# Kernel optimization log

Hardware: AMD Instinct MI355X
Metric: run time of the kernel (lower is better)

The kernel has to match this reference:

```python
import jax, jax.numpy as jnp
import numpy as np

N_NODES = 100000
N_EDGES = 1250000
D_IN = 64
D_HID = 64
N_CLS = 40


def setup_inputs() -> dict:
    key = jax.random.key(0)
    ks = jax.random.split(key, 8)
    x = jax.random.normal(ks[0], (N_NODES, D_IN), dtype=jnp.float32)
    edge_index = jax.random.randint(ks[1], (2, N_EDGES), 0, N_NODES, dtype=jnp.int64)
    s = 1.0 / np.sqrt(D_IN)
    W1_l = jax.random.normal(ks[2], (D_IN, D_HID), dtype=jnp.float32) * s
    W1_r = jax.random.normal(ks[3], (D_IN, D_HID), dtype=jnp.float32) * s
    b1 = jnp.zeros((D_HID,), dtype=jnp.float32)
    s2 = 1.0 / np.sqrt(D_HID)
    W2_l = jax.random.normal(ks[4], (D_HID, N_CLS), dtype=jnp.float32) * s2
    W2_r = jax.random.normal(ks[5], (D_HID, N_CLS), dtype=jnp.float32) * s2
    b2 = jnp.zeros((N_CLS,), dtype=jnp.float32)
    return {"x": x, "edge_index": edge_index, "W1_l": W1_l, "b1": b1,
            "W1_r": W1_r, "W2_l": W2_l, "b2": b2, "W2_r": W2_r}


def _sage_conv(h, src, dst, n_nodes, W_l, b, W_r):
    # mean-aggregate neighbor features: out[i] = mean_{(j->i)} h[j]
    msg = h[src]                                             # [E, d] gather
    agg = jax.ops.segment_sum(msg, dst, num_segments=n_nodes)  # [N, d] scatter-add
    deg = jax.ops.segment_sum(jnp.ones_like(dst, dtype=h.dtype), dst,
                              num_segments=n_nodes)
    agg = agg / jnp.maximum(deg, 1.0)[:, None]
    # lin_l(aggregated, bias) + lin_r(root, no bias)
    return agg @ W_l + b + h @ W_r


def reference(x, edge_index, W1_l, b1, W1_r, W2_l, b2, W2_r):
    n = x.shape[0]
    src, dst = edge_index[0], edge_index[1]
    h = jax.nn.relu(_sage_conv(x, src, dst, n, W1_l, b1, W1_r))
    # dropout is identity in eval mode (training=False)
    h = _sage_conv(h, src, dst, n, W2_l, b2, W2_r)
    return jax.nn.log_softmax(h, axis=1)
```

## Files before the change

kernel.cpp:

```cpp
#include <hip/hip_runtime.h>
#include <hip/hip_bf16.h>
#include <math.h>

#define N_NODES 100000
#define N_EDGES 1250000
#define D_IN    64
#define D_HID   64
#define N_CLS   40

#define NBUCK      500
#define BUCK_NODES 200
#define BUCK_CAP   2944
#define NBLK_STAGE 512
#define ELL_W      44

typedef unsigned int uint;
typedef __attribute__((ext_vector_type(8))) short bf16x8;
typedef __attribute__((ext_vector_type(4))) float f32x4;

static __device__ __forceinline__ uint pack_bf16x2(float a, float b) {
    unsigned short ua = __builtin_bit_cast(unsigned short, __float2bfloat16(a));
    unsigned short ub = __builtin_bit_cast(unsigned short, __float2bfloat16(b));
    return (uint)ua | ((uint)ub << 16);
}
static __device__ __forceinline__ short f2bf(float f) {
    return (short)__builtin_bit_cast(unsigned short, __float2bfloat16(f));
}

__global__ __launch_bounds__(256) void bucket_stage(
    const int* __restrict__ src, const int* __restrict__ dst,
    int* __restrict__ bucketCnt, uint* __restrict__ staged, int n_edges)
{
    __shared__ int cntB[NBUCK], offB[NBUCK], gbase[NBUCK];
    const int per = (n_edges + NBLK_STAGE - 1) / NBLK_STAGE;
    const int e0 = blockIdx.x * per;
    const int e1 = (e0 + per < n_edges) ? e0 + per : n_edges;
    for (int i = threadIdx.x; i < NBUCK; i += 256) { cntB[i] = 0; offB[i] = 0; }
    __syncthreads();
    for (int e = e0 + threadIdx.x; e < e1; e += 256)
        atomicAdd(&cntB[dst[e] / BUCK_NODES], 1);
    __syncthreads();
    for (int i = threadIdx.x; i < NBUCK; i += 256) {
        int c = cntB[i];
        gbase[i] = c ? atomicAdd(&bucketCnt[i], c) : 0;
    }
    __syncthreads();
    for (int e = e0 + threadIdx.x; e < e1; e += 256) {
        int d = dst[e];
        int s = src[e];
        int b = d / BUCK_NODES;
        int pos = gbase[b] + atomicAdd(&offB[b], 1);
        if (pos < BUCK_CAP)
            staged[(size_t)b * BUCK_CAP + pos] =
                (uint)s | ((uint)(d - b * BUCK_NODES) << 17);
    }
}

__global__ __launch_bounds__(256) void ell_fill(
    const uint* __restrict__ staged, const int* __restrict__ bucketCnt,
    int* __restrict__ cnt, int* __restrict__ slots)
{
    __shared__ int lcnt[BUCK_NODES];
    const int b = blockIdx.x;
    const int node0 = b * BUCK_NODES;
    for (int i = threadIdx.x; i < BUCK_NODES; i += 256) lcnt[i] = 0;
    __syncthreads();
    int total = bucketCnt[b];
    if (total > BUCK_CAP) total = BUCK_CAP;
    const uint* sp = staged + (size_t)b * BUCK_CAP;
    for (int i = threadIdx.x; i < total; i += 256) {
        uint v = sp[i];
        int off = (int)(v >> 17);
        int pos = atomicAdd(&lcnt[off], 1);
        if (pos < ELL_W)
            slots[(size_t)(node0 + off) * ELL_W + pos] = (int)(v & 0x1FFFFu);
    }
    __syncthreads();
    for (int i = threadIdx.x; i < BUCK_NODES; i += 256) {
        int node = node0 + i;
        if (node < N_NODES) cnt[node] = lcnt[i];
    }
}

__global__ __launch_bounds__(256, 3) void gemm1_mfma(
    const float* __restrict__ x,
    const float* __restrict__ W_l, const float* __restrict__ W_r,
    const float* __restrict__ b,
    __hip_bfloat16* __restrict__ y1, __hip_bfloat16* __restrict__ r1,
    int ntiles)
{
    const int lane = threadIdx.x & 63;
    const int m = lane & 15;
    const int q = lane >> 4;

    bf16x8 bfrag[8][2];
    float  biasv[4];
    #pragma unroll
    for (int t = 0; t < 8; ++t) {
        const float* Wsrc = (t < 4) ? W_l : W_r;
        const int c = t * 16 + m - ((t < 4) ? 0 : 64);
        #pragma unroll
        for (int ks = 0; ks < 2; ++ks) {
            bf16x8 f;
            #pragma unroll
            for (int j = 0; j < 8; ++j)
                f[j] = f2bf(Wsrc[(ks * 32 + q * 8 + j) * 64 + c]);
            bfrag[t][ks] = f;
        }
    }
    #pragma unroll
    for (int t = 0; t < 4; ++t) biasv[t] = b[t * 16 + m];

    int wid = blockIdx.x * 4 + (threadIdx.x >> 6);
    const int nw = gridDim.x * 4;
    for (int tile = wid; tile < ntiles; tile += nw) {
        const int node0 = tile * 16;
        const float* xrow = x + (size_t)(node0 + m) * 64 + q * 8;
        bf16x8 afrag[2];
        #pragma unroll
        for (int ks = 0; ks < 2; ++ks) {
            float4 f0 = *(const float4*)(xrow + ks * 32);
            float4 f1 = *(const float4*)(xrow + ks * 32 + 4);
            bf16x8 a;
            a[0] = f2bf(f0.x); a[1] = f2bf(f0.y); a[2] = f2bf(f0.z); a[3] = f2bf(f0.w);
            a[4] = f2bf(f1.x); a[5] = f2bf(f1.y); a[6] = f2bf(f1.z); a[7] = f2bf(f1.w);
            afrag[ks] = a;
        }
        f32x4 acc[8];
        #pragma unroll
        for (int t = 0; t < 8; ++t) acc[t] = (f32x4){0.f, 0.f, 0.f, 0.f};
        #pragma unroll
        for (int ks = 0; ks < 2; ++ks) {
            #pragma unroll
            for (int t = 0; t < 8; ++t)
                acc[t] = __builtin_amdgcn_mfma_f32_16x16x32_bf16(
                    afrag[ks], bfrag[t][ks], acc[t], 0, 0, 0);
        }
        #pragma unroll
        for (int t = 0; t < 8; ++t) {
            #pragma unroll
            for (int r = 0; r < 4; ++r) {
                const size_t row = (size_t)(node0 + q * 4 + r);
                if (t < 4)
                    y1[row * 64 + t * 16 + m] = __float2bfloat16(acc[t][r]);
                else
                    r1[row * 64 + (t - 4) * 16 + m] =
                        __float2bfloat16(acc[t][r] + biasv[t - 4]);
            }
        }
    }
}

__global__ __launch_bounds__(256, 3) void gemm2_mfma(
    const __hip_bfloat16* __restrict__ h,
    const float* __restrict__ W_l, const float* __restrict__ W_r,
    const float* __restrict__ b,
    __hip_bfloat16* __restrict__ y2, __hip_bfloat16* __restrict__ r2,
    int ntiles)
{
    const int lane = threadIdx.x & 63;
    const int m = lane & 15;
    const int q = lane >> 4;

    bf16x8 bfrag[5][2];
    float  biasv[5];
    #pragma unroll
    for (int t = 0; t < 5; ++t) {
        const int g = t * 16 + m;
        const float* Wsrc = (g < N_CLS) ? W_l : W_r;
        const int c = (g < N_CLS) ? g : g - N_CLS;
        #pragma unroll
        for (int ks = 0; ks < 2; ++ks) {
            bf16x8 f;
            #pragma unroll
            for (int j = 0; j < 8; ++j)
                f[j] = f2bf(Wsrc[(ks * 32 + q * 8 + j) * N_CLS + c]);
            bfrag[t][ks] = f;
        }
        biasv[t] = (g >= N_CLS) ? b[g - N_CLS] : 0.0f;
    }

    int wid = blockIdx.x * 4 + (threadIdx.x >> 6);
    const int nw = gridDim.x * 4;
    for (int tile = wid; tile < ntiles; tile += nw) {
        const int node0 = tile * 16;
        const __hip_bfloat16* hrow = h + (size_t)(node0 + m) * 64 + q * 8;
        bf16x8 afrag[2];
        afrag[0] = *(const bf16x8*)(hrow);
        afrag[1] = *(const bf16x8*)(hrow + 32);
        f32x4 acc[5];
        #pragma unroll
        for (int t = 0; t < 5; ++t) acc[t] = (f32x4){0.f, 0.f, 0.f, 0.f};
        #pragma unroll
        for (int ks = 0; ks < 2; ++ks) {
            #pragma unroll
            for (int t = 0; t < 5; ++t)
                acc[t] = __builtin_amdgcn_mfma_f32_16x16x32_bf16(
                    afrag[ks], bfrag[t][ks], acc[t], 0, 0, 0);
        }
        #pragma unroll
        for (int t = 0; t < 5; ++t) {
            const int g = t * 16 + m;
            #pragma unroll
            for (int r = 0; r < 4; ++r) {
                const size_t row = (size_t)(node0 + q * 4 + r);
                float v = acc[t][r] + biasv[t];
                if (g < N_CLS) y2[row * N_CLS + g] = __float2bfloat16(v);
                else           r2[row * N_CLS + (g - N_CLS)] = __float2bfloat16(v);
            }
        }
    }
}

__global__ __launch_bounds__(256, 8) void gather1(
    const __hip_bfloat16* __restrict__ y1,
    const int* __restrict__ cnt, const int* __restrict__ slots,
    __hip_bfloat16* __restrict__ h,
    int n_nodes)
{
    const int lane = threadIdx.x & 63;
    const int q4  = (lane >> 4) * 4;
    const int pre = (lane & 15) * 8;
    const char* y1c = (const char*)y1;

    const int wave = blockIdx.x * 4 + (threadIdx.x >> 6);
    const int nw   = gridDim.x * 4;

    for (int node = wave; node < n_nodes; node += nw) {
        const int degr = cnt[node];
        const int degc = degr < ELL_W ? degr : ELL_W;
        int idx = slots[node * ELL_W + lane];
        if (lane >= degc) idx = n_nodes;
        float a0 = 0.f, a1 = 0.f, a2 = 0.f, a3 = 0.f;
        const int groups = (degc + 15) & ~15;
        for (int e = 0; e < groups; e += 16) {
            int sel0 = __builtin_amdgcn_ds_bpermute(e * 4      + q4, idx);
            int sel1 = __builtin_amdgcn_ds_bpermute(e * 4 + 16 + q4, idx);
            int sel2 = __builtin_amdgcn_ds_bpermute(e * 4 + 32 + q4, idx);
            int sel3 = __builtin_amdgcn_ds_bpermute(e * 4 + 48 + q4, idx);
            uint2 d0 = *(const uint2*)(y1c + ((size_t)(uint)sel0 * 128u + (uint)pre));
            uint2 d1 = *(const uint2*)(y1c + ((size_t)(uint)sel1 * 128u + (uint)pre));
            uint2 d2 = *(const uint2*)(y1c + ((size_t)(uint)sel2 * 128u + (uint)pre));
            uint2 d3 = *(const uint2*)(y1c + ((size_t)(uint)sel3 * 128u + (uint)pre));
            a0 += __uint_as_float(d0.x << 16) + __uint_as_float(d1.x << 16)
                + __uint_as_float(d2.x << 16) + __uint_as_float(d3.x << 16);
            a1 += __uint_as_float(d0.x & 0xffff0000u) + __uint_as_float(d1.x & 0xffff0000u)
                + __uint_as_float(d2.x & 0xffff0000u) + __uint_as_float(d3.x & 0xffff0000u);
            a2 += __uint_as_float(d0.y << 16) + __uint_as_float(d1.y << 16)
                + __uint_as_float(d2.y << 16) + __uint_as_float(d3.y << 16);
            a3 += __uint_as_float(d0.y & 0xffff0000u) + __uint_as_float(d1.y & 0xffff0000u)
                + __uint_as_float(d2.y & 0xffff0000u) + __uint_as_float(d3.y & 0xffff0000u);
        }
        a0 += __shfl_xor(a0, 16); a0 += __shfl_xor(a0, 32);
        a1 += __shfl_xor(a1, 16); a1 += __shfl_xor(a1, 32);
        a2 += __shfl_xor(a2, 16); a2 += __shfl_xor(a2, 32);
        a3 += __shfl_xor(a3, 16); a3 += __shfl_xor(a3, 32);

        uint2 rr = *(const uint2*)((const char*)h + ((size_t)node * 128u + (uint)pre));
        float r0  = __uint_as_float(rr.x << 16);
        float r1v = __uint_as_float(rr.x & 0xffff0000u);
        float r2v = __uint_as_float(rr.y << 16);
        float r3  = __uint_as_float(rr.y & 0xffff0000u);

        float inv = 1.0f / (float)(degr > 1 ? degr : 1);
        float v0 = a0 * inv + r0;  v0 = v0 > 0.f ? v0 : 0.f;
        float v1 = a1 * inv + r1v; v1 = v1 > 0.f ? v1 : 0.f;
        float v2 = a2 * inv + r2v; v2 = v2 > 0.f ? v2 : 0.f;
        float v3 = a3 * inv + r3;  v3 = v3 > 0.f ? v3 : 0.f;

        if (lane < 16) {
            uint2 o;
            o.x = pack_bf16x2(v0, v1);
            o.y = pack_bf16x2(v2, v3);
            *(uint2*)((char*)h + ((size_t)node * 128u + (uint)pre)) = o;
        }
    }
}

__global__ __launch_bounds__(256, 8) void gather2(
    const __hip_bfloat16* __restrict__ y2,
    const __hip_bfloat16* __restrict__ r2,
    const int* __restrict__ cnt, const int* __restrict__ slots,
    float* __restrict__ out, int n_nodes)
{
    const int lane  = threadIdx.x & 63;
    const int lpair = lane & 31;
    const int p2    = (lane >> 5) * 4;
    const int pre2  = (lpair < 20 ? lpair : 19) * 4;
    const char* y2c = (const char*)y2;

    const int wave = blockIdx.x * 4 + (threadIdx.x >> 6);
    const int nw   = gridDim.x * 4;

    for (int node = wave; node < n_nodes; node += nw) {
        const int degr = cnt[node];
        const int degc = degr < ELL_W ? degr : ELL_W;
        int idx = slots[node * ELL_W + lane];
        if (lane >= degc) idx = n_nodes;
        float a0 = 0.f, a1 = 0.f;
        const int groups = (degc + 7) & ~7;
        for (int e = 0; e < groups; e += 8) {
            int sel0 = __builtin_amdgcn_ds_bpermute(e * 4      + p2, idx);
            int sel1 = __builtin_amdgcn_ds_bpermute(e * 4 +  8 + p2, idx);
            int sel2 = __builtin_amdgcn_ds_bpermute(e * 4 + 16 + p2, idx);
            int sel3 = __builtin_amdgcn_ds_bpermute(e * 4 + 24 + p2, idx);
            uint d0 = *(const uint*)(y2c + ((size_t)(uint)sel0 * 80u + (uint)pre2));
            uint d1 = *(const uint*)(y2c + ((size_t)(uint)sel1 * 80u + (uint)pre2));
            uint d2 = *(const uint*)(y2c + ((size_t)(uint)sel2 * 80u + (uint)pre2));
            uint d3 = *(const uint*)(y2c + ((size_t)(uint)sel3 * 80u + (uint)pre2));
            a0 += __uint_as_float(d0 << 16) + __uint_as_float(d1 << 16)
                + __uint_as_float(d2 << 16) + __uint_as_float(d3 << 16);
            a1 += __uint_as_float(d0 & 0xffff0000u) + __uint_as_float(d1 & 0xffff0000u)
                + __uint_as_float(d2 & 0xffff0000u) + __uint_as_float(d3 & 0xffff0000u);
        }
        a0 += __shfl_xor(a0, 32);
        a1 += __shfl_xor(a1, 32);

        uint rr = *(const uint*)((const char*)r2 + ((size_t)node * 80u + (uint)pre2));
        float r0 = __uint_as_float(rr << 16);
        float r1 = __uint_as_float(rr & 0xffff0000u);

        float inv = 1.0f / (float)(degr > 1 ? degr : 1);
        float l0 = a0 * inv + r0;
        float l1 = a1 * inv + r1;
        if (lpair >= 20) { l0 = -INFINITY; l1 = -INFINITY; }

        float m = fmaxf(l0, l1);
        #pragma unroll
        for (int off = 16; off > 0; off >>= 1)
            m = fmaxf(m, __shfl_xor(m, off));
        float ex = (lpair < 20) ? (expf(l0 - m) + expf(l1 - m)) : 0.0f;
        #pragma unroll
        for (int off = 16; off > 0; off >>= 1)
            ex += __shfl_xor(ex, off);
        float lg = m + logf(ex);
        if (lane < 20) {
            float2 o = make_float2(l0 - lg, l1 - lg);
            *(float2*)(out + (size_t)node * N_CLS + lpair * 2) = o;
        }
    }
}

extern "C" void kernel_launch(void* const* d_in, const int* in_sizes, int n_in,
                              void* d_out, int out_size, void* d_ws, size_t ws_size,
                              hipStream_t stream)
{
    (void)in_sizes; (void)n_in; (void)out_size; (void)ws_size;

    const float* x    = (const float*)d_in[0];
    const int*   ei   = (const int*)d_in[1];
    const float* W1_l = (const float*)d_in[2];
    const float* b1   = (const float*)d_in[3];
    const float* W1_r = (const float*)d_in[4];
    const float* W2_l = (const float*)d_in[5];
    const float* b2   = (const float*)d_in[6];
    const float* W2_r = (const float*)d_in[7];
    float* out = (float*)d_out;

    const int* src = ei;
    const int* dst = ei + N_EDGES;

    char* ws = (char*)d_ws;
    int*            cnt       = (int*)(ws);
    int*            bucketCnt = (int*)(ws + 400000);
    int*            slots     = (int*)(ws + (1u << 20));
    __hip_bfloat16* y1        = (__hip_bfloat16*)(ws + 19922944u);
    __hip_bfloat16* y2        = (__hip_bfloat16*)(ws + 19922944u);
    __hip_bfloat16* h         = (__hip_bfloat16*)(ws + 34603008u);
    uint*           staged    = (uint*)(ws + 48234496u);
    __hip_bfloat16* r2        = (__hip_bfloat16*)(ws + 48234496u);

    hipMemsetAsync(bucketCnt, 0, NBUCK * sizeof(int), stream);
    bucket_stage<<<NBLK_STAGE, 256, 0, stream>>>(src, dst, bucketCnt, staged, N_EDGES);
    ell_fill<<<NBUCK, 256, 0, stream>>>(staged, bucketCnt, cnt, slots);

    const int ntiles = N_NODES / 16;

    hipMemsetAsync(y1 + (size_t)N_NODES * 64, 0, 64 * sizeof(__hip_bfloat16), stream);
    gemm1_mfma<<<1024, 256, 0, stream>>>(x, W1_l, W1_r, b1, y1, h, ntiles);
    gather1<<<2048, 256, 0, stream>>>(y1, cnt, slots, h, N_NODES);

    hipMemsetAsync(y2 + (size_t)N_NODES * N_CLS, 0, N_CLS * sizeof(__hip_bfloat16), stream);
    gemm2_mfma<<<1024, 256, 0, stream>>>(h, W2_l, W2_r, b2, y2, r2, ntiles);
    gather2<<<2048, 256, 0, stream>>>(y2, r2, cnt, slots, out, N_NODES);
}
```

Baseline: 213.7 us.

## Merge bucket staging with GEMM1, drop memsets, prefetch next node's ELL slots

Bucket staging and the first-layer GEMM now run as one launch, with different blocks taking each role, so the two independent phases overlap and a launch is removed. The two padding-row memsets are replaced by in-kernel zero stores. The gather loops now load the next node's degree and slot indices before processing the current node, hiding that load latency. Costs: the fused kernel runs under launch bounds (256,3) for the staging blocks too, and the prefetch uses extra registers.

Result: faster. 203.0 us (-5.0%).

```diff
diff --git a/kernel.cpp b/kernel.cpp
--- a/kernel.cpp
+++ b/kernel.cpp
@@ -12,6 +12,7 @@
 #define BUCK_NODES 200
 #define BUCK_CAP   2944
 #define NBLK_STAGE 512
+#define NBLK_GEMM1 1024
 #define ELL_W      44
 
 typedef unsigned int uint;
@@ -27,32 +28,106 @@
     return (short)__builtin_bit_cast(unsigned short, __float2bfloat16(f));
 }
 
-__global__ __launch_bounds__(256) void bucket_stage(
+__global__ __launch_bounds__(256, 3) void stage_and_gemm1(
     const int* __restrict__ src, const int* __restrict__ dst,
-    int* __restrict__ bucketCnt, uint* __restrict__ staged, int n_edges)
+    int* __restrict__ bucketCnt, uint* __restrict__ staged,
+    const float* __restrict__ x,
+    const float* __restrict__ W_l, const float* __restrict__ W_r,
+    const float* __restrict__ b,
+    __hip_bfloat16* __restrict__ y1, __hip_bfloat16* __restrict__ r1,
+    int ntiles)
 {
     __shared__ int cntB[NBUCK], offB[NBUCK], gbase[NBUCK];
-    const int per = (n_edges + NBLK_STAGE - 1) / NBLK_STAGE;
-    const int e0 = blockIdx.x * per;
-    const int e1 = (e0 + per < n_edges) ? e0 + per : n_edges;
-    for (int i = threadIdx.x; i < NBUCK; i += 256) { cntB[i] = 0; offB[i] = 0; }
-    __syncthreads();
-    for (int e = e0 + threadIdx.x; e < e1; e += 256)
-        atomicAdd(&cntB[dst[e] / BUCK_NODES], 1);
-    __syncthreads();
-    for (int i = threadIdx.x; i < NBUCK; i += 256) {
-        int c = cntB[i];
-        gbase[i] = c ? atomicAdd(&bucketCnt[i], c) : 0;
-    }
-    __syncthreads();
-    for (int e = e0 + threadIdx.x; e < e1; e += 256) {
-        int d = dst[e];
-        int s = src[e];
-        int b = d / BUCK_NODES;
-        int pos = gbase[b] + atomicAdd(&offB[b], 1);
-        if (pos < BUCK_CAP)
-            staged[(size_t)b * BUCK_CAP + pos] =
-                (uint)s | ((uint)(d - b * BUCK_NODES) << 17);
+
+    if (blockIdx.x < NBLK_STAGE) {
+        const int per = (N_EDGES + NBLK_STAGE - 1) / NBLK_STAGE;
+        const int e0 = blockIdx.x * per;
+        const int e1 = (e0 + per < N_EDGES) ? e0 + per : N_EDGES;
+        for (int i = threadIdx.x; i < NBUCK; i += 256) { cntB[i] = 0; offB[i] = 0; }
+        __syncthreads();
+        for (int e = e0 + threadIdx.x; e < e1; e += 256)
+            atomicAdd(&cntB[dst[e] / BUCK_NODES], 1);
+        __syncthreads();
+        for (int i = threadIdx.x; i < NBUCK; i += 256) {
+            int c = cntB[i];
+            gbase[i] = c ? atomicAdd(&bucketCnt[i], c) : 0;
+        }
+        __syncthreads();
+        for (int e = e0 + threadIdx.x; e < e1; e += 256) {
+            int d = dst[e];
+            int s = src[e];
+            int bk = d / BUCK_NODES;
+            int pos = gbase[bk] + atomicAdd(&offB[bk], 1);
+            if (pos < BUCK_CAP)
+                staged[(size_t)bk * BUCK_CAP + pos] =
+                    (uint)s | ((uint)(d - bk * BUCK_NODES) << 17);
+        }
+        return;
+    }
+
+    const int gbid = blockIdx.x - NBLK_STAGE;
+    if (gbid == 0 && threadIdx.x < 64)
+        y1[(size_t)N_NODES * 64 + threadIdx.x] = __float2bfloat16(0.0f);
+
+    const int lane = threadIdx.x & 63;
+    const int m = lane & 15;
+    const int q = lane >> 4;
+
+    bf16x8 bfrag[8][2];
+    float  biasv[4];
+    #pragma unroll
+    for (int t = 0; t < 8; ++t) {
+        const float* Wsrc = (t < 4) ? W_l : W_r;
+        const int c = t * 16 + m - ((t < 4) ? 0 : 64);
+        #pragma unroll
+        for (int ks = 0; ks < 2; ++ks) {
+            bf16x8 f;
+            #pragma unroll
+            for (int j = 0; j < 8; ++j)
+                f[j] = f2bf(Wsrc[(ks * 32 + q * 8 + j) * 64 + c]);
+            bfrag[t][ks] = f;
+        }
+    }
+    #pragma unroll
+    for (int t = 0; t < 4; ++t) biasv[t] = b[t * 16 + m];
+
+    int wid = gbid * 4 + (threadIdx.x >> 6);
+    const int nw = NBLK_GEMM1 * 4;
+    for (int tile = wid; tile < ntiles; tile += nw) {
+        const int node0 = tile * 16;
+        const float* xrow = x + (size_t)(node0 + m) * 64 + q * 8;
+        bf16x8 afrag[2];
+        #pragma unroll
+        for (int ks = 0; ks < 2; ++ks) {
+            float4 f0 = *(const float4*)(xrow + ks * 32);
+            float4 f1 = *(const float4*)(xrow + ks * 32 + 4);
+            bf16x8 a;
+            a[0] = f2bf(f0.x); a[1] = f2bf(f0.y); a[2] = f2bf(f0.z); a[3] = f2bf(f0.w);
+            a[4] = f2bf(f1.x); a[5] = f2bf(f1.y); a[6] = f2bf(f1.z); a[7] = f2bf(f1.w);
+            afrag[ks] = a;
+        }
+        f32x4 acc[8];
+        #pragma unroll
+        for (int t = 0; t < 8; ++t) acc[t] = (f32x4){0.f, 0.f, 0.f, 0.f};
+        #pragma unroll
+        for (int ks = 0; ks < 2; ++ks) {
+            #pragma unroll
+            for (int t = 0; t < 8; ++t)
+                acc[t] = __builtin_amdgcn_mfma_f32_16x16x32_bf16(
+                    afrag[ks], bfrag[t][ks], acc[t], 0, 0, 0);
+        }
+        #pragma unroll
+        for (int t = 0; t < 8; ++t) {
+            #pragma unroll
+            for (int r = 0; r < 4; ++r) {
+                const size_t row = (size_t)(node0 + q * 4 + r);
+                if (t < 4)
+                    y1[row * 64 + t * 16 + m] = __float2bfloat16(acc[t][r]);
+                else
+                    r1[row * 64 + (t - 4) * 16 + m] =
+                        __float2bfloat16(acc[t][r] + biasv[t - 4]);
+            }
+        }
     }
 }
 
@@ -82,75 +157,6 @@
     }
 }
 
-__global__ __launch_bounds__(256, 3) void gemm1_mfma(
-    const float* __restrict__ x,
-    const float* __restrict__ W_l, const float* __restrict__ W_r,
-    const float* __restrict__ b,
-    __hip_bfloat16* __restrict__ y1, __hip_bfloat16* __restrict__ r1,
-    int ntiles)
-{
-    const int lane = threadIdx.x & 63;
-    const int m = lane & 15;
-    const int q = lane >> 4;
-
-    bf16x8 bfrag[8][2];
-    float  biasv[4];
-    #pragma unroll
-    for (int t = 0; t < 8; ++t) {
-        const float* Wsrc = (t < 4) ? W_l : W_r;
-        const int c = t * 16 + m - ((t < 4) ? 0 : 64);
-        #pragma unroll
-        for (int ks = 0; ks < 2; ++ks) {
-            bf16x8 f;
-            #pragma unroll
-            for (int j = 0; j < 8; ++j)
-                f[j] = f2bf(Wsrc[(ks * 32 + q * 8 + j) * 64 + c]);
-            bfrag[t][ks] = f;
-        }
-    }
-    #pragma unroll
-    for (int t = 0; t < 4; ++t) biasv[t] = b[t * 16 + m];
-
-    int wid = blockIdx.x * 4 + (threadIdx.x >> 6);
-    const int nw = gridDim.x * 4;
-    for (int tile = wid; tile < ntiles; tile += nw) {
-        const int node0 = tile * 16;
-        const float* xrow = x + (size_t)(node0 + m) * 64 + q * 8;
-        bf16x8 afrag[2];
-        #pragma unroll
-        for (int ks = 0; ks < 2; ++ks) {
-            float4 f0 = *(const float4*)(xrow + ks * 32);
-            float4 f1 = *(const float4*)(xrow + ks * 32 + 4);
-            bf16x8 a;
-            a[0] = f2bf(f0.x); a[1] = f2bf(f0.y); a[2] = f2bf(f0.z); a[3] = f2bf(f0.w);
-            a[4] = f2bf(f1.x); a[5] = f2bf(f1.y); a[6] = f2bf(f1.z); a[7] = f2bf(f1.w);
-            afrag[ks] = a;
-        }
-        f32x4 acc[8];
-        #pragma unroll
-        for (int t = 0; t < 8; ++t) acc[t] = (f32x4){0.f, 0.f, 0.f, 0.f};
-        #pragma unroll
-        for (int ks = 0; ks < 2; ++ks) {
-            #pragma unroll
-            for (int t = 0; t < 8; ++t)
-                acc[t] = __builtin_amdgcn_mfma_f32_16x16x32_bf16(
-                    afrag[ks], bfrag[t][ks], acc[t], 0, 0, 0);
-        }
-        #pragma unroll
-        for (int t = 0; t < 8; ++t) {
-            #pragma unroll
-            for (int r = 0; r < 4; ++r) {
-                const size_t row = (size_t)(node0 + q * 4 + r);
-                if (t < 4)
-                    y1[row * 64 + t * 16 + m] = __float2bfloat16(acc[t][r]);
-                else
-                    r1[row * 64 + (t - 4) * 16 + m] =
-                        __float2bfloat16(acc[t][r] + biasv[t - 4]);
-            }
-        }
-    }
-}
-
 __global__ __launch_bounds__(256, 3) void gemm2_mfma(
     const __hip_bfloat16* __restrict__ h,
     const float* __restrict__ W_l, const float* __restrict__ W_r,
@@ -158,6 +164,9 @@
     __hip_bfloat16* __restrict__ y2, __hip_bfloat16* __restrict__ r2,
     int ntiles)
 {
+    if (blockIdx.x == 0 && threadIdx.x < N_CLS)
+        y2[(size_t)N_NODES * N_CLS + threadIdx.x] = __float2bfloat16(0.0f);
+
     const int lane = threadIdx.x & 63;
     const int m = lane & 15;
     const int q = lane >> 4;
@@ -226,11 +235,21 @@
     const int wave = blockIdx.x * 4 + (threadIdx.x >> 6);
     const int nw   = gridDim.x * 4;
 
-    for (int node = wave; node < n_nodes; node += nw) {
-        const int degr = cnt[node];
+    int node = wave;
+    if (node >= n_nodes) return;
+    int degr = cnt[node];
+    int idxv = slots[node * ELL_W + lane];
+
+    for (;;) {
+        const int nnode = node + nw;
+        int ndeg = 0, nidx = 0;
+        if (nnode < n_nodes) {
+            ndeg = cnt[nnode];
+            nidx = slots[nnode * ELL_W + lane];
+        }
+
         const int degc = degr < ELL_W ? degr : ELL_W;
-        int idx = slots[node * ELL_W + lane];
-        if (lane >= degc) idx = n_nodes;
+        int idx = (lane >= degc) ? n_nodes : idxv;
         float a0 = 0.f, a1 = 0.f, a2 = 0.f, a3 = 0.f;
         const int groups = (degc + 15) & ~15;
         for (int e = 0; e < groups; e += 16) {
@@ -274,6 +293,9 @@
             o.y = pack_bf16x2(v2, v3);
             *(uint2*)((char*)h + ((size_t)node * 128u + (uint)pre)) = o;
         }
+
+        if (nnode >= n_nodes) break;
+        node = nnode; degr = ndeg; idxv = nidx;
     }
 }
 
@@ -292,11 +314,21 @@
     const int wave = blockIdx.x * 4 + (threadIdx.x >> 6);
     const int nw   = gridDim.x * 4;
 
-    for (int node = wave; node < n_nodes; node += nw) {
-        const int degr = cnt[node];
+    int node = wave;
+    if (node >= n_nodes) return;
+    int degr = cnt[node];
+    int idxv = slots[node * ELL_W + lane];
+
+    for (;;) {
+        const int nnode = node + nw;
+        int ndeg = 0, nidx = 0;
+        if (nnode < n_nodes) {
+            ndeg = cnt[nnode];
+            nidx = slots[nnode * ELL_W + lane];
+        }
+
         const int degc = degr < ELL_W ? degr : ELL_W;
-        int idx = slots[node * ELL_W + lane];
-        if (lane >= degc) idx = n_nodes;
+        int idx = (lane >= degc) ? n_nodes : idxv;
         float a0 = 0.f, a1 = 0.f;
         const int groups = (degc + 7) & ~7;
         for (int e = 0; e < groups; e += 8) {
@@ -338,6 +370,9 @@
             float2 o = make_float2(l0 - lg, l1 - lg);
             *(float2*)(out + (size_t)node * N_CLS + lpair * 2) = o;
         }
+
+        if (nnode >= n_nodes) break;
+        node = nnode; degr = ndeg; idxv = nidx;
     }
 }
 
@@ -370,17 +405,17 @@
     uint*           staged    = (uint*)(ws + 48234496u);
     __hip_bfloat16* r2        = (__hip_bfloat16*)(ws + 48234496u);
 
+    const int ntiles = N_NODES / 16;
+
     hipMemsetAsync(bucketCnt, 0, NBUCK * sizeof(int), stream);
-    bucket_stage<<<NBLK_STAGE, 256, 0, stream>>>(src, dst, bucketCnt, staged, N_EDGES);
+    stage_and_gemm1<<<NBLK_STAGE + NBLK_GEMM1, 256, 0, stream>>>(
+        src, dst, bucketCnt, staged, x, W1_l, W1_r, b1, y1, h, ntiles);
+
     ell_fill<<<NBUCK, 256, 0, stream>>>(staged, bucketCnt, cnt, slots);
 
-    const int ntiles = N_NODES / 16;
-
-    hipMemsetAsync(y1 + (size_t)N_NODES * 64, 0, 64 * sizeof(__hip_bfloat16), stream);
-    gemm1_mfma<<<1024, 256, 0, stream>>>(x, W1_l, W1_r, b1, y1, h, ntiles);
     gather1<<<2048, 256, 0, stream>>>(y1, cnt, slots, h, N_NODES);
 
-    hipMemsetAsync(y2 + (size_t)N_NODES * N_CLS, 0, N_CLS * sizeof(__hip_bfloat16), stream);
     gemm2_mfma<<<1024, 256, 0, stream>>>(h, W2_l, W2_r, b2, y2, r2, ntiles);
+
     gather2<<<2048, 256, 0, stream>>>(y2, r2, cnt, slots, out, N_NODES);
 }
```
